# Kernel optimization log

Hardware: AMD Instinct MI355X
Metric: run time of the kernel (lower is better)

Reference implementation:

```python
import jax, jax.numpy as jnp
import numpy as np

B, T, C = 2, 2048, 1280
H, D = 10, 128  # n_head, head_dim (n_kv_head == n_head, so no repeat)
EPS = 1e-5
NEG = -1e9


def setup_inputs() -> dict:
    key = jax.random.key(0)
    ks = jax.random.split(key, 7)
    s = 0.02
    return {
        "x": jax.random.normal(ks[0], (B, T, C), jnp.float32),
        "cos": jax.random.normal(ks[1], (1, 1, T, D // 2), jnp.float32),
        "sin": jax.random.normal(ks[2], (1, 1, T, D // 2), jnp.float32),
        "Wq": jax.random.normal(ks[3], (C, C), jnp.float32) * s,
        "Wk": jax.random.normal(ks[4], (C, C), jnp.float32) * s,
        "Wv": jax.random.normal(ks[5], (C, C), jnp.float32) * s,
        "Wproj": jax.random.normal(ks[6], (C, C), jnp.float32) * s,
    }


def _rope(x, cos, sin):
    # x: [b,h,t,d]; split last dim in half
    x1, x2 = jnp.split(x, 2, axis=-1)
    y1 = x1 * cos + x2 * sin
    y2 = -x1 * sin + x2 * cos
    return jnp.concatenate([y1, y2], axis=-1)


def _rms_norm(x):
    mean = jnp.mean(x * x, axis=-1, keepdims=True)
    return x / jnp.sqrt(mean + EPS)


def reference(x, cos, sin, Wq, Wk, Wv, Wproj):
    b, t, c = x.shape
    # nn.Linear: y = x @ W.T; weights stored [out, in]
    q = (x @ Wq.T).reshape(b, t, H, D).transpose(0, 2, 1, 3)  # [b,h,t,d]
    k = (x @ Wk.T).reshape(b, t, H, D).transpose(0, 2, 1, 3)
    v = (x @ Wv.T).reshape(b, t, H, D).transpose(0, 2, 1, 3)
    q = _rms_norm(_rope(q, cos, sin))
    k = _rms_norm(_rope(k, cos, sin))
    scale = 1.0 / jnp.sqrt(jnp.float32(D))
    scores = jnp.einsum("bhqd,bhkd->bhqk", q, k) * scale
    mask = jnp.triu(jnp.ones((t, t), scores.dtype), k=1)  # 1 above diagonal
    scores = scores + mask * NEG
    attn = jax.nn.softmax(scores, axis=-1)
    y = jnp.einsum("bhqk,bhkd->bhqd", attn, v)
    y = y.transpose(0, 2, 1, 3).reshape(b, t, c)
    return y @ Wproj.T
```

## Files before the change

### kernel.cpp

```cpp
#include <hip/hip_runtime.h>
#include <hip/hip_bf16.h>

#define B_ 2
#define T_ 2048
#define C_ 1280
#define H_ 10
#define D_ 128
#define BT_ (B_*T_)

typedef __hip_bfloat16 bf16;
typedef __attribute__((ext_vector_type(8))) short short8;
typedef __attribute__((ext_vector_type(4))) float f32x4;

__device__ __forceinline__ float bf2f(bf16 v){ return __bfloat162float(v); }
__device__ __forceinline__ bf16  f2bf(float v){ return __float2bfloat16(v); }
__device__ __forceinline__ void stv(bf16* p, float v){ *p = f2bf(v); }
__device__ __forceinline__ void stv(float* p, float v){ *p = v; }

struct alignas(8) bf4 { bf16 a,b,c,d; };

__device__ __forceinline__ void gl2lds(const bf16* g, bf16* l) {
    __builtin_amdgcn_global_load_lds(
        (const __attribute__((address_space(1))) void*)g,
        (__attribute__((address_space(3))) void*)l,
        16, 0, 0);
}

__global__ __launch_bounds__(256)
void cvt(const float* __restrict__ s, bf16* __restrict__ d)
{
    const int i = (blockIdx.x*256 + threadIdx.x)*4;
    const float4 v = *(const float4*)(s + i);
    bf4 o = { f2bf(v.x), f2bf(v.y), f2bf(v.z), f2bf(v.w) };
    *(bf4*)(d + i) = o;
}

__global__ __launch_bounds__(256)
void cvtW(const float* __restrict__ s0, const float* __restrict__ s1,
          const float* __restrict__ s2, const float* __restrict__ s3,
          bf16* __restrict__ d)
{
    const int w = blockIdx.y;
    const float* s = (w==0)?s0:(w==1)?s1:(w==2)?s2:s3;
    const int i = (blockIdx.x*256 + threadIdx.x)*4;
    const float4 v = *(const float4*)(s + i);
    bf4 o = { f2bf(v.x), f2bf(v.y), f2bf(v.z), f2bf(v.w) };
    *(bf4*)(d + (size_t)w*C_*C_ + i) = o;
}

template <typename OT>
__global__ __launch_bounds__(256,4)
void gemm_nt(const bf16* __restrict__ A, const bf16* __restrict__ Wb,
             OT* __restrict__ O0, OT* __restrict__ O1, OT* __restrict__ O2)
{
    __shared__ __align__(16) bf16 As[128*64];
    __shared__ __align__(16) bf16 Bs[128*64];
    const int z = blockIdx.z;
    const bf16* Wm = Wb + (size_t)z*C_*C_;
    OT*         Om = (z==0) ? O0 : (z==1) ? O1 : O2;
    const int wave = threadIdx.x >> 6;
    const int lane = threadIdx.x & 63;
    const int l15 = lane & 15, quad = lane >> 4;
    const int row0 = blockIdx.x*128;
    const int col0 = blockIdx.y*128;
    const int wm = (wave>>1)*64, wn = (wave&1)*64;
    const int srow = lane >> 3;
    const int scol = (lane & 7)*8;

    const f32x4 fzero = {0.f,0.f,0.f,0.f};
    f32x4 acc[4][4];
    #pragma unroll
    for (int i=0;i<4;i++)
        #pragma unroll
        for (int j=0;j<4;j++) acc[i][j] = fzero;

    const bf16* Ag = A  + (size_t)(row0 + wave*32 + srow)*C_ + scol;
    const bf16* Bg = Wm + (size_t)(col0 + wave*32 + srow)*C_ + scol;
    bf16* Al = As + (wave*32)*64;
    bf16* Bl = Bs + (wave*32)*64;

    for (int k0 = 0; k0 < C_; k0 += 64) {
        __syncthreads();
        #pragma unroll
        for (int i=0;i<4;i++){
            gl2lds(Ag + (size_t)i*8*C_ + k0, Al + i*8*64);
            gl2lds(Bg + (size_t)i*8*C_ + k0, Bl + i*8*64);
        }
        asm volatile("s_waitcnt vmcnt(0)" ::: "memory");
        __syncthreads();
        #pragma unroll
        for (int h=0; h<2; ++h) {
            short8 af[4], bfv[4];
            #pragma unroll
            for (int mt=0; mt<4; ++mt) af[mt]  = *(const short8*)(As + (wm + mt*16 + l15)*64 + h*32 + quad*8);
            #pragma unroll
            for (int nt=0; nt<4; ++nt) bfv[nt] = *(const short8*)(Bs + (wn + nt*16 + l15)*64 + h*32 + quad*8);
            #pragma unroll
            for (int mt=0; mt<4; ++mt)
                #pragma unroll
                for (int nt=0; nt<4; ++nt)
                    acc[mt][nt] = __builtin_amdgcn_mfma_f32_16x16x32_bf16(af[mt], bfv[nt], acc[mt][nt], 0,0,0);
        }
    }
    #pragma unroll
    for (int mt=0; mt<4; ++mt)
        #pragma unroll
        for (int nt=0; nt<4; ++nt)
            #pragma unroll
            for (int r=0; r<4; ++r)
                stv(&Om[(size_t)(row0 + wm + mt*16 + quad*4 + r)*C_ + col0 + wn + nt*16 + l15], acc[mt][nt][r]);
}

__global__ __launch_bounds__(256,4)
void gemm_nt_m64(const bf16* __restrict__ A, const bf16* __restrict__ Wm,
                 float* __restrict__ Om)
{
    __shared__ __align__(16) bf16 As[64*64];
    __shared__ __align__(16) bf16 Bs[128*64];
    const int wave = threadIdx.x >> 6;
    const int lane = threadIdx.x & 63;
    const int l15 = lane & 15, quad = lane >> 4;
    const int row0 = blockIdx.x*64;
    const int col0 = blockIdx.y*128;
    const int wm = (wave>>1)*32, wn = (wave&1)*64;
    const int srow = lane >> 3;
    const int scol = (lane & 7)*8;

    const f32x4 fzero = {0.f,0.f,0.f,0.f};
    f32x4 acc[2][4];
    #pragma unroll
    for (int i=0;i<2;i++)
        #pragma unroll
        for (int j=0;j<4;j++) acc[i][j] = fzero;

    const bf16* Ag = A  + (size_t)(row0 + wave*16 + srow)*C_ + scol;
    const bf16* Bg = Wm + (size_t)(col0 + wave*32 + srow)*C_ + scol;
    bf16* Al = As + (wave*16)*64;
    bf16* Bl = Bs + (wave*32)*64;

    for (int k0 = 0; k0 < C_; k0 += 64) {
        __syncthreads();
        #pragma unroll
        for (int i=0;i<2;i++)
            gl2lds(Ag + (size_t)i*8*C_ + k0, Al + i*8*64);
        #pragma unroll
        for (int i=0;i<4;i++)
            gl2lds(Bg + (size_t)i*8*C_ + k0, Bl + i*8*64);
        asm volatile("s_waitcnt vmcnt(0)" ::: "memory");
        __syncthreads();
        #pragma unroll
        for (int h=0; h<2; ++h) {
            short8 af[2], bfv[4];
            #pragma unroll
            for (int mt=0; mt<2; ++mt) af[mt]  = *(const short8*)(As + (wm + mt*16 + l15)*64 + h*32 + quad*8);
            #pragma unroll
            for (int nt=0; nt<4; ++nt) bfv[nt] = *(const short8*)(Bs + (wn + nt*16 + l15)*64 + h*32 + quad*8);
            #pragma unroll
            for (int mt=0; mt<2; ++mt)
                #pragma unroll
                for (int nt=0; nt<4; ++nt)
                    acc[mt][nt] = __builtin_amdgcn_mfma_f32_16x16x32_bf16(af[mt], bfv[nt], acc[mt][nt], 0,0,0);
        }
    }
    #pragma unroll
    for (int mt=0; mt<2; ++mt)
        #pragma unroll
        for (int nt=0; nt<4; ++nt)
            #pragma unroll
            for (int r=0; r<4; ++r)
                Om[(size_t)(row0 + wm + mt*16 + quad*4 + r)*C_ + col0 + wn + nt*16 + l15] = acc[mt][nt][r];
}

__global__ __launch_bounds__(256)
void rope_rms(bf16* __restrict__ q, bf16* __restrict__ k,
              const float* __restrict__ cosp, const float* __restrict__ sinp)
{
    const int wave = threadIdx.x >> 6, lane = threadIdx.x & 63;
    const long rb = (long)blockIdx.x*4 + wave;
    const int h = (int)(rb % H_);
    const long bt = rb / H_;
    const int t = (int)(bt % T_);
    bf16* buf = blockIdx.y ? k : q;
    const size_t base = (size_t)bt*C_ + (size_t)h*D_;
    float x1 = bf2f(buf[base + lane]);
    float x2 = bf2f(buf[base + 64 + lane]);
    float c  = cosp[(size_t)t*64 + lane];
    float s  = sinp[(size_t)t*64 + lane];
    float y1 =  x1*c + x2*s;
    float y2 = -x1*s + x2*c;
    float ss = y1*y1 + y2*y2;
    #pragma unroll
    for (int off=1; off<64; off<<=1) ss += __shfl_xor(ss, off);
    float sc = rsqrtf(ss*(1.0f/128.0f) + 1e-5f);
    buf[base + lane]      = f2bf(y1*sc);
    buf[base + 64 + lane] = f2bf(y2*sc);
}

__global__ __launch_bounds__(256)
void vtrans(const bf16* __restrict__ V, bf16* __restrict__ Vt)
{
    __shared__ float st[64][65];
    const int tid = threadIdx.x;
    const int bh = blockIdx.z;
    const int b = bh / H_, h = bh % H_;
    const int t0 = blockIdx.x*64, d0 = blockIdx.y*64;
    #pragma unroll
    for (int i=0;i<16;i++){
        int e = tid + i*256;
        int r = e >> 6, dd = e & 63;
        st[r][dd] = bf2f(V[(size_t)(b*T_ + t0 + r)*C_ + h*D_ + d0 + dd]);
    }
    __syncthreads();
    #pragma unroll
    for (int i=0;i<16;i++){
        int e = tid + i*256;
        int dd = e >> 6, r = e & 63;
        Vt[((size_t)bh*D_ + d0 + dd)*T_ + t0 + r] = f2bf(st[r][dd]);
    }
}

#define M0_ 11.3137085f
__global__ __launch_bounds__(256,3)
void attn(const bf16* __restrict__ Q, const bf16* __restrict__ K,
          const bf16* __restrict__ Vt, bf16* __restrict__ Y,
          bf16* __restrict__ opart, float* __restrict__ lpart)
{
    __shared__ __align__(16) bf16 kbuf[64*128];
    __shared__ __align__(16) bf16 vbuf[128*64];
    __shared__ __align__(16) bf16 ptile[4][16*72];
    const int wave = threadIdx.x >> 6, lane = threadIdx.x & 63;
    const int l15 = lane & 15, quad = lane >> 4;
    const int bh = blockIdx.x % 20;
    const int u  = blockIdx.x / 20;
    int m, seg;
    if (u < 32)      { m = 31 - (u>>2); seg = u & 3; }
    else if (u < 56) { const int v2 = u-32; m = 23 - v2/3; seg = v2%3; }
    else if (u < 72) { const int v2 = u-56; m = 15 - (v2>>1); seg = v2&1; }
    else             { m = 7 - (u-72); seg = 0; }
    const int b = bh / H_, h = bh % H_;
    const int t0 = m*64;
    const int nch = m + 1;
    const int cbeg = seg*8;
    const int cend = min(cbeg+8, nch);
    const bool direct = (m < 8);
    const size_t base = (size_t)b*T_*C_ + (size_t)h*D_;
    const bf16* Kbh = K + base;
    const bf16* Vbh = Vt + (size_t)bh*D_*T_;
    const int t0w = t0 + wave*16;
    const float scale = 0.08838834764831845f;
    bf16* pt = ptile[wave];

    short8 qa[4];
    {
        const bf16* qp = Q + base + (size_t)(t0w + l15)*C_ + quad*8;
        #pragma unroll
        for (int kb4=0; kb4<4; ++kb4) qa[kb4] = *(const short8*)(qp + kb4*32);
    }
    const f32x4 fzero = {0.f,0.f,0.f,0.f};
    f32x4 o[8];
    #pragma unroll
    for (int dt=0; dt<8; ++dt) o[dt] = fzero;
    float lp[4] = {0.f,0.f,0.f,0.f};

    const int vr_off = lane >> 3;
    const int vu     = lane & 7;

    for (int ch=cbeg; ch<cend; ++ch) {
        const int k0 = ch*64;
        __syncthreads();
        #pragma unroll
        for (int j=0;j<4;j++){
            const int row = wave*16 + j*4 + quad;
            const int ug  = (l15 - row) & 15;
            gl2lds(Kbh + (size_t)(k0 + row)*C_ + ug*8, &kbuf[(wave*16 + j*4)*128]);
        }
        #pragma unroll
        for (int j=0;j<4;j++){
            const int r  = wave*32 + j*8 + vr_off;
            const int ug = (vu - r) & 7;
            gl2lds(Vbh + (size_t)r*T_ + k0 + ug*8, &vbuf[(wave*32 + j*8)*64]);
        }
        asm volatile("s_waitcnt vmcnt(0)" ::: "memory");
        __syncthreads();

        f32x4 sc4[4];
        #pragma unroll
        for (int c=0;c<4;c++) sc4[c] = fzero;
        #pragma unroll
        for (int c=0;c<4;c++){
            short8 kf[4];
            #pragma unroll
            for (int kb4=0; kb4<4; ++kb4) {
                const int up = (kb4*4 + quad + l15) & 15;
                kf[kb4] = *(const short8*)(&kbuf[(c*16 + l15)*128 + up*8]);
            }
            #pragma unroll
            for (int kb4=0; kb4<4; ++kb4)
                sc4[c] = __builtin_amdgcn_mfma_f32_16x16x32_bf16(qa[kb4], kf[kb4], sc4[c], 0,0,0);
        }
        const bool lastc = (ch == nch-1);
        #pragma unroll
        for (int r=0; r<4; ++r) {
            const int rt = t0w + quad*4 + r;
            float v[4];
            #pragma unroll
            for (int c=0;c<4;c++) v[c] = sc4[c][r]*scale;
            if (lastc) {
                #pragma unroll
                for (int c=0;c<4;c++) if (k0 + c*16 + l15 > rt) v[c] = -1e30f;
            }
            float p[4];
            #pragma unroll
            for (int c=0;c<4;c++) p[c] = __expf(v[c] - M0_);
            lp[r] += (p[0]+p[1]) + (p[2]+p[3]);
            #pragma unroll
            for (int c=0;c<4;c++) pt[(quad*4+r)*72 + c*16 + l15] = f2bf(p[c]);
        }
        asm volatile("s_waitcnt lgkmcnt(0)" ::: "memory");
        short8 pa[2];
        #pragma unroll
        for (int ks=0; ks<2; ++ks)
            pa[ks] = *(const short8*)(pt + l15*72 + ks*32 + quad*8);
        #pragma unroll
        for (int dt=0; dt<8; ++dt) {
            #pragma unroll
            for (int ks=0; ks<2; ++ks) {
                const int up = (ks*4 + quad + l15) & 7;
                short8 vF = *(const short8*)(&vbuf[(dt*16 + l15)*64 + up*8]);
                o[dt] = __builtin_amdgcn_mfma_f32_16x16x32_bf16(pa[ks], vF, o[dt], 0,0,0);
            }
        }
    }

    #pragma unroll
    for (int r=0; r<4; ++r) {
        #pragma unroll
        for (int off=1; off<16; off<<=1) lp[r] += __shfl_xor(lp[r], off);
    }
    if (direct) {
        float li[4];
        #pragma unroll
        for (int r=0; r<4; ++r) li[r] = 1.0f/lp[r];
        #pragma unroll
        for (int dt=0; dt<8; ++dt)
            #pragma unroll
            for (int r=0; r<4; ++r)
                Y[base + (size_t)(t0w + quad*4 + r)*C_ + dt*16 + l15] = f2bf(o[dt][r]*li[r]);
    } else {
        const int off = (m<16) ? (m-8)*2 : (m<24) ? 16 + (m-16)*3 : 40 + (m-24)*4;
        const int slot = bh*72 + off + seg;
        bf16* ob = opart + (size_t)slot*8192 + (wave*16)*128;
        #pragma unroll
        for (int dt=0; dt<8; ++dt)
            #pragma unroll
            for (int r=0; r<4; ++r)
                ob[(quad*4+r)*128 + dt*16 + l15] = f2bf(o[dt][r]);
        if (l15 == 0) {
            #pragma unroll
            for (int r=0; r<4; ++r) lpart[(size_t)slot*64 + wave*16 + quad*4 + r] = lp[r];
        }
    }
}

__global__ __launch_bounds__(256)
void combineN(const bf16* __restrict__ opart, const float* __restrict__ lpart,
              bf16* __restrict__ Y)
{
    const int tt = blockIdx.x;
    const int bh = tt / 24;
    const int m  = 8 + (tt % 24);
    const int nseg = (m + 8) >> 3;
    const int off = (m<16) ? (m-8)*2 : (m<24) ? 16 + (m-16)*3 : 40 + (m-24)*4;
    const int slot0 = bh*72 + off;
    const int b = bh / H_, h = bh % H_;
    const int row = threadIdx.x >> 2;
    const int d0 = (threadIdx.x & 3)*32;
    float l = 0.f;
    for (int s=0; s<nseg; ++s) l += lpart[(size_t)(slot0+s)*64 + row];
    const float li = 1.0f/l;
    float acc[32];
    #pragma unroll
    for (int e=0;e<32;e++) acc[e] = 0.f;
    for (int s=0; s<nseg; ++s) {
        const bf16* p = opart + (size_t)(slot0+s)*8192 + row*128 + d0;
        #pragma unroll
        for (int e=0;e<32;e++) acc[e] += bf2f(p[e]);
    }
    bf16 ov[32];
    #pragma unroll
    for (int e=0;e<32;e++) ov[e] = f2bf(acc[e]*li);
    bf16* yp = Y + (size_t)b*T_*C_ + (size_t)(m*64+row)*C_ + (size_t)h*D_ + d0;
    #pragma unroll
    for (int v=0; v<4; ++v) *(short8*)(yp + v*8) = *(const short8*)(&ov[v*8]);
}

extern "C" void kernel_launch(void* const* d_in, const int* in_sizes, int n_in,
                              void* d_out, int out_size, void* d_ws, size_t ws_size,
                              hipStream_t stream)
{
    const float* x    = (const float*)d_in[0];
    const float* cosp = (const float*)d_in[1];
    const float* sinp = (const float*)d_in[2];
    const float* Wq   = (const float*)d_in[3];
    const float* Wk   = (const float*)d_in[4];
    const float* Wv   = (const float*)d_in[5];
    const float* Wp   = (const float*)d_in[6];
    float* out = (float*)d_out;

    const size_t NE = (size_t)BT_ * C_;
    const size_t NW = (size_t)C_ * C_;
    bf16* xb = (bf16*)d_ws;
    bf16* wb = xb + NE;
    bf16* q  = wb + 4*NW;
    bf16* k  = q + NE;
    bf16* v  = k + NE;
    bf16* y  = v + NE;
    bf16* vT = y + NE;
    bf16* op = vT + NE;
    float* lpart = (float*)(op + (size_t)1440*8192);

    cvt<<<dim3(NE/1024), 256, 0, stream>>>(x, xb);
    cvtW<<<dim3(NW/1024, 4), 256, 0, stream>>>(Wq, Wk, Wv, Wp, wb);
    gemm_nt<bf16><<<dim3(BT_/128, C_/128, 3), 256, 0, stream>>>(xb, wb, q, k, v);
    rope_rms<<<dim3(BT_*H_/4, 2), 256, 0, stream>>>(q, k, cosp, sinp);
    vtrans<<<dim3(T_/64, D_/64, B_*H_), 256, 0, stream>>>(v, vT);
    attn<<<dim3(1600), 256, 0, stream>>>(q, k, vT, y, op, lpart);
    combineN<<<dim3(480), 256, 0, stream>>>(op, lpart, y);
    gemm_nt_m64<<<dim3(BT_/64, C_/128), 256, 0, stream>>>(y, wb + 3*NW, out);
}
```

Measured before the change: 246.4 us.

## Replace QKV GEMM with 256x256 double-buffered swizzled tile kernel

New measurement: 249.2 us. Within noise of the previous version (+1.1%).

```diff
diff --git a/kernel.cpp b/kernel.cpp
--- a/kernel.cpp
+++ b/kernel.cpp
@@ -14,8 +14,6 @@
 
 __device__ __forceinline__ float bf2f(bf16 v){ return __bfloat162float(v); }
 __device__ __forceinline__ bf16  f2bf(float v){ return __float2bfloat16(v); }
-__device__ __forceinline__ void stv(bf16* p, float v){ *p = f2bf(v); }
-__device__ __forceinline__ void stv(float* p, float v){ *p = v; }
 
 struct alignas(8) bf4 { bf16 a,b,c,d; };
 
@@ -48,67 +46,140 @@
     *(bf4*)(d + (size_t)w*C_*C_ + i) = o;
 }
 
-template <typename OT>
-__global__ __launch_bounds__(256,4)
-void gemm_nt(const bf16* __restrict__ A, const bf16* __restrict__ Wb,
-             OT* __restrict__ O0, OT* __restrict__ O1, OT* __restrict__ O2)
-{
-    __shared__ __align__(16) bf16 As[128*64];
-    __shared__ __align__(16) bf16 Bs[128*64];
+__global__ __launch_bounds__(512,2)
+void gemm256(const bf16* __restrict__ A, const bf16* __restrict__ Wb,
+             bf16* __restrict__ O0, bf16* __restrict__ O1, bf16* __restrict__ O2)
+{
+    __shared__ __align__(16) bf16 As[2][256*64];
+    __shared__ __align__(16) bf16 Bs[2][256*64];
     const int z = blockIdx.z;
     const bf16* Wm = Wb + (size_t)z*C_*C_;
-    OT*         Om = (z==0) ? O0 : (z==1) ? O1 : O2;
-    const int wave = threadIdx.x >> 6;
+    bf16*       Om = (z==0) ? O0 : (z==1) ? O1 : O2;
+    const int w    = threadIdx.x >> 6;
     const int lane = threadIdx.x & 63;
     const int l15 = lane & 15, quad = lane >> 4;
-    const int row0 = blockIdx.x*128;
-    const int col0 = blockIdx.y*128;
-    const int wm = (wave>>1)*64, wn = (wave&1)*64;
-    const int srow = lane >> 3;
-    const int scol = (lane & 7)*8;
+    const int warp_m = w >> 2, warp_n = w & 3;
+    const int row0 = blockIdx.x*256;
+    const int col0 = blockIdx.y*256;
+
+    const int sr = lane >> 3;
+    const int ug = ((lane & 7) - sr) & 7;
+    const bf16* Ag = A  + (size_t)(row0 + w*32 + sr)*C_ + ug*8;
+    const bf16* Bg = Wm + (size_t)(col0 + w*32 + sr)*C_ + ug*8;
 
     const f32x4 fzero = {0.f,0.f,0.f,0.f};
-    f32x4 acc[4][4];
-    #pragma unroll
-    for (int i=0;i<4;i++)
+    f32x4 acc[8][4];
+    #pragma unroll
+    for (int i=0;i<8;i++)
         #pragma unroll
         for (int j=0;j<4;j++) acc[i][j] = fzero;
 
-    const bf16* Ag = A  + (size_t)(row0 + wave*32 + srow)*C_ + scol;
-    const bf16* Bg = Wm + (size_t)(col0 + wave*32 + srow)*C_ + scol;
-    bf16* Al = As + (wave*32)*64;
-    bf16* Bl = Bs + (wave*32)*64;
-
-    for (int k0 = 0; k0 < C_; k0 += 64) {
+    const int NT = C_/64;
+
+    #pragma unroll
+    for (int tt=0; tt<2; ++tt) {
+        #pragma unroll
+        for (int j=0;j<4;j++){
+            gl2lds(Ag + (size_t)j*8*C_ + tt*64, &As[tt][(w*32 + j*8)*64]);
+            gl2lds(Bg + (size_t)j*8*C_ + tt*64, &Bs[tt][(w*32 + j*8)*64]);
+        }
+    }
+
+    const int arow = warp_m*128 + l15;
+    const int brow = warp_n*64  + l15;
+
+    for (int t=0; t<NT; ++t) {
+        const int cur = t & 1;
+        if (t < NT-1) asm volatile("s_waitcnt vmcnt(8)" ::: "memory");
+        else          asm volatile("s_waitcnt vmcnt(0)" ::: "memory");
         __syncthreads();
+        const bf16* Ab = &As[cur][0];
+        const bf16* Bb = &Bs[cur][0];
+
+        short8 a[4][2], bfr[4][2];
         #pragma unroll
         for (int i=0;i<4;i++){
-            gl2lds(Ag + (size_t)i*8*C_ + k0, Al + i*8*64);
-            gl2lds(Bg + (size_t)i*8*C_ + k0, Bl + i*8*64);
-        }
-        asm volatile("s_waitcnt vmcnt(0)" ::: "memory");
+            const int r = arow + i*16;
+            #pragma unroll
+            for (int h=0;h<2;h++)
+                a[i][h] = *(const short8*)(Ab + r*64 + ((h*4 + quad + r)&7)*8);
+        }
+        #pragma unroll
+        for (int n=0;n<2;n++){
+            const int r = brow + n*16;
+            #pragma unroll
+            for (int h=0;h<2;h++)
+                bfr[n][h] = *(const short8*)(Bb + r*64 + ((h*4 + quad + r)&7)*8);
+        }
+        __builtin_amdgcn_s_setprio(1);
+        #pragma unroll
+        for (int i=0;i<4;i++)
+            #pragma unroll
+            for (int n=0;n<2;n++)
+                #pragma unroll
+                for (int h=0;h<2;h++)
+                    acc[i][n] = __builtin_amdgcn_mfma_f32_16x16x32_bf16(a[i][h], bfr[n][h], acc[i][n], 0,0,0);
+        __builtin_amdgcn_s_setprio(0);
+        #pragma unroll
+        for (int n=2;n<4;n++){
+            const int r = brow + n*16;
+            #pragma unroll
+            for (int h=0;h<2;h++)
+                bfr[n][h] = *(const short8*)(Bb + r*64 + ((h*4 + quad + r)&7)*8);
+        }
+        __builtin_amdgcn_s_setprio(1);
+        #pragma unroll
+        for (int i=0;i<4;i++)
+            #pragma unroll
+            for (int n=2;n<4;n++)
+                #pragma unroll
+                for (int h=0;h<2;h++)
+                    acc[i][n] = __builtin_amdgcn_mfma_f32_16x16x32_bf16(a[i][h], bfr[n][h], acc[i][n], 0,0,0);
+        __builtin_amdgcn_s_setprio(0);
+        #pragma unroll
+        for (int i=0;i<4;i++){
+            const int r = arow + (4+i)*16;
+            #pragma unroll
+            for (int h=0;h<2;h++)
+                a[i][h] = *(const short8*)(Ab + r*64 + ((h*4 + quad + r)&7)*8);
+        }
+        __builtin_amdgcn_s_setprio(1);
+        #pragma unroll
+        for (int i=0;i<4;i++)
+            #pragma unroll
+            for (int n=2;n<4;n++)
+                #pragma unroll
+                for (int h=0;h<2;h++)
+                    acc[4+i][n] = __builtin_amdgcn_mfma_f32_16x16x32_bf16(a[i][h], bfr[n][h], acc[4+i][n], 0,0,0);
+        __builtin_amdgcn_s_setprio(0);
+        __builtin_amdgcn_s_setprio(1);
+        #pragma unroll
+        for (int i=0;i<4;i++)
+            #pragma unroll
+            for (int n=0;n<2;n++)
+                #pragma unroll
+                for (int h=0;h<2;h++)
+                    acc[4+i][n] = __builtin_amdgcn_mfma_f32_16x16x32_bf16(a[i][h], bfr[n][h], acc[4+i][n], 0,0,0);
+        __builtin_amdgcn_s_setprio(0);
+
         __syncthreads();
-        #pragma unroll
-        for (int h=0; h<2; ++h) {
-            short8 af[4], bfv[4];
-            #pragma unroll
-            for (int mt=0; mt<4; ++mt) af[mt]  = *(const short8*)(As + (wm + mt*16 + l15)*64 + h*32 + quad*8);
-            #pragma unroll
-            for (int nt=0; nt<4; ++nt) bfv[nt] = *(const short8*)(Bs + (wn + nt*16 + l15)*64 + h*32 + quad*8);
-            #pragma unroll
-            for (int mt=0; mt<4; ++mt)
-                #pragma unroll
-                for (int nt=0; nt<4; ++nt)
-                    acc[mt][nt] = __builtin_amdgcn_mfma_f32_16x16x32_bf16(af[mt], bfv[nt], acc[mt][nt], 0,0,0);
-        }
-    }
-    #pragma unroll
-    for (int mt=0; mt<4; ++mt)
+        if (t+2 < NT) {
+            #pragma unroll
+            for (int j=0;j<4;j++){
+                gl2lds(Ag + (size_t)j*8*C_ + (t+2)*64, &As[cur][(w*32 + j*8)*64]);
+                gl2lds(Bg + (size_t)j*8*C_ + (t+2)*64, &Bs[cur][(w*32 + j*8)*64]);
+            }
+        }
+    }
+
+    #pragma unroll
+    for (int mt=0; mt<8; ++mt)
         #pragma unroll
         for (int nt=0; nt<4; ++nt)
             #pragma unroll
             for (int r=0; r<4; ++r)
-                stv(&Om[(size_t)(row0 + wm + mt*16 + quad*4 + r)*C_ + col0 + wn + nt*16 + l15], acc[mt][nt][r]);
+                Om[(size_t)(row0 + warp_m*128 + mt*16 + quad*4 + r)*C_ + col0 + warp_n*64 + nt*16 + l15]
+                    = f2bf(acc[mt][nt][r]);
 }
 
 __global__ __launch_bounds__(256,4)
@@ -271,14 +342,14 @@
         #pragma unroll
         for (int j=0;j<4;j++){
             const int row = wave*16 + j*4 + quad;
-            const int ug  = (l15 - row) & 15;
-            gl2lds(Kbh + (size_t)(k0 + row)*C_ + ug*8, &kbuf[(wave*16 + j*4)*128]);
+            const int ugk = (l15 - row) & 15;
+            gl2lds(Kbh + (size_t)(k0 + row)*C_ + ugk*8, &kbuf[(wave*16 + j*4)*128]);
         }
         #pragma unroll
         for (int j=0;j<4;j++){
             const int r  = wave*32 + j*8 + vr_off;
-            const int ug = (vu - r) & 7;
-            gl2lds(Vbh + (size_t)r*T_ + k0 + ug*8, &vbuf[(wave*32 + j*8)*64]);
+            const int ugv = (vu - r) & 7;
+            gl2lds(Vbh + (size_t)r*T_ + k0 + ugv*8, &vbuf[(wave*32 + j*8)*64]);
         }
         asm volatile("s_waitcnt vmcnt(0)" ::: "memory");
         __syncthreads();
@@ -421,7 +492,7 @@
 
     cvt<<<dim3(NE/1024), 256, 0, stream>>>(x, xb);
     cvtW<<<dim3(NW/1024, 4), 256, 0, stream>>>(Wq, Wk, Wv, Wp, wb);
-    gemm_nt<bf16><<<dim3(BT_/128, C_/128, 3), 256, 0, stream>>>(xb, wb, q, k, v);
+    gemm256<<<dim3(BT_/256, C_/256, 3), 512, 0, stream>>>(xb, wb, q, k, v);
     rope_rms<<<dim3(BT_*H_/4, 2), 256, 0, stream>>>(q, k, cosp, sinp);
     vtrans<<<dim3(T_/64, D_/64, B_*H_), 256, 0, stream>>>(v, vT);
     attn<<<dim3(1600), 256, 0, stream>>>(q, k, vT, y, op, lpart);
```

## Fuse RoPE, RMS norm and V transpose into QKV GEMM epilogue

Applied to the files above, without the earlier changes.

Result: faster. 232.3 us (-5.7%).

```diff
diff --git a/kernel.cpp b/kernel.cpp
--- a/kernel.cpp
+++ b/kernel.cpp
@@ -14,8 +14,6 @@
 
 __device__ __forceinline__ float bf2f(bf16 v){ return __bfloat162float(v); }
 __device__ __forceinline__ bf16  f2bf(float v){ return __float2bfloat16(v); }
-__device__ __forceinline__ void stv(bf16* p, float v){ *p = f2bf(v); }
-__device__ __forceinline__ void stv(float* p, float v){ *p = v; }
 
 struct alignas(8) bf4 { bf16 a,b,c,d; };
 
@@ -27,37 +25,38 @@
 }
 
 __global__ __launch_bounds__(256)
-void cvt(const float* __restrict__ s, bf16* __restrict__ d)
-{
-    const int i = (blockIdx.x*256 + threadIdx.x)*4;
+void cvtall(const float* __restrict__ x,  const float* __restrict__ w0,
+            const float* __restrict__ w1, const float* __restrict__ w2,
+            const float* __restrict__ w3, bf16* __restrict__ xb,
+            bf16* __restrict__ wb)
+{
+    int bid = blockIdx.x;
+    const float* s; bf16* d; int i;
+    if (bid < 5120) {
+        s = x; d = xb; i = (bid*256 + threadIdx.x)*4;
+    } else {
+        bid -= 5120;
+        const int w = bid / 1600;
+        const int r = bid % 1600;
+        s = (w==0)?w0:(w==1)?w1:(w==2)?w2:w3;
+        d = wb + (size_t)w*C_*C_;
+        i = (r*256 + threadIdx.x)*4;
+    }
     const float4 v = *(const float4*)(s + i);
     bf4 o = { f2bf(v.x), f2bf(v.y), f2bf(v.z), f2bf(v.w) };
     *(bf4*)(d + i) = o;
 }
 
-__global__ __launch_bounds__(256)
-void cvtW(const float* __restrict__ s0, const float* __restrict__ s1,
-          const float* __restrict__ s2, const float* __restrict__ s3,
-          bf16* __restrict__ d)
-{
-    const int w = blockIdx.y;
-    const float* s = (w==0)?s0:(w==1)?s1:(w==2)?s2:s3;
-    const int i = (blockIdx.x*256 + threadIdx.x)*4;
-    const float4 v = *(const float4*)(s + i);
-    bf4 o = { f2bf(v.x), f2bf(v.y), f2bf(v.z), f2bf(v.w) };
-    *(bf4*)(d + (size_t)w*C_*C_ + i) = o;
-}
-
-template <typename OT>
 __global__ __launch_bounds__(256,4)
-void gemm_nt(const bf16* __restrict__ A, const bf16* __restrict__ Wb,
-             OT* __restrict__ O0, OT* __restrict__ O1, OT* __restrict__ O2)
-{
-    __shared__ __align__(16) bf16 As[128*64];
-    __shared__ __align__(16) bf16 Bs[128*64];
+void gemm_qkv(const bf16* __restrict__ A, const bf16* __restrict__ Wb,
+              bf16* __restrict__ q, bf16* __restrict__ k, bf16* __restrict__ vT,
+              const float* __restrict__ cosp, const float* __restrict__ sinp)
+{
+    __shared__ __align__(16) bf16 smem[17408];
+    bf16* As = smem;
+    bf16* Bs = smem + 8192;
     const int z = blockIdx.z;
     const bf16* Wm = Wb + (size_t)z*C_*C_;
-    OT*         Om = (z==0) ? O0 : (z==1) ? O1 : O2;
     const int wave = threadIdx.x >> 6;
     const int lane = threadIdx.x & 63;
     const int l15 = lane & 15, quad = lane >> 4;
@@ -102,13 +101,92 @@
                     acc[mt][nt] = __builtin_amdgcn_mfma_f32_16x16x32_bf16(af[mt], bfv[nt], acc[mt][nt], 0,0,0);
         }
     }
-    #pragma unroll
-    for (int mt=0; mt<4; ++mt)
-        #pragma unroll
-        for (int nt=0; nt<4; ++nt)
-            #pragma unroll
-            for (int r=0; r<4; ++r)
-                stv(&Om[(size_t)(row0 + wm + mt*16 + quad*4 + r)*C_ + col0 + wn + nt*16 + l15], acc[mt][nt][r]);
+
+    __syncthreads();
+    if (z == 2) {
+        const int RS = 136;
+        #pragma unroll
+        for (int mt=0; mt<4; ++mt)
+            #pragma unroll
+            for (int nt=0; nt<4; ++nt) {
+                bf4 pk = { f2bf(acc[mt][nt][0]), f2bf(acc[mt][nt][1]),
+                           f2bf(acc[mt][nt][2]), f2bf(acc[mt][nt][3]) };
+                *(bf4*)(smem + (wn + nt*16 + l15)*RS + wm + mt*16 + quad*4) = pk;
+            }
+        __syncthreads();
+        const int b    = row0 >> 11;
+        const int trow = row0 & 2047;
+        const int h    = col0 >> 7;
+        bf16* vbase = vT + (size_t)(b*H_ + h)*D_*T_ + trow;
+        const int g   = threadIdx.x >> 4;
+        const int l16 = threadIdx.x & 15;
+        #pragma unroll
+        for (int i=0;i<8;i++){
+            const int col = i*16 + g;
+            *(short8*)(vbase + (size_t)col*T_ + l16*8) = *(const short8*)(smem + col*RS + l16*8);
+        }
+    } else {
+        bf16* dst = z ? k : q;
+        bf16* my  = smem + wave*4096;
+        bf16* pr  = smem + (wave^1)*4096;
+        float* ssb = (float*)(smem + 16384);
+        #pragma unroll
+        for (int mt=0; mt<4; ++mt)
+            #pragma unroll
+            for (int nt=0; nt<4; ++nt) {
+                bf4 pk = { f2bf(acc[mt][nt][0]), f2bf(acc[mt][nt][1]),
+                           f2bf(acc[mt][nt][2]), f2bf(acc[mt][nt][3]) };
+                *(bf4*)(my + ((((mt*4+nt)*4+quad)*16+l15)<<2)) = pk;
+            }
+        __syncthreads();
+        const bool upper = (wave & 1);
+        float ss[4][4];
+        #pragma unroll
+        for (int mt=0; mt<4; ++mt) {
+            #pragma unroll
+            for (int r=0; r<4; ++r) ss[mt][r] = 0.f;
+            #pragma unroll
+            for (int nt=0; nt<4; ++nt) {
+                const bf4 pv = *(const bf4*)(pr + ((((mt*4+nt)*4+quad)*16+l15)<<2));
+                const float p[4] = { bf2f(pv.a), bf2f(pv.b), bf2f(pv.c), bf2f(pv.d) };
+                const int j = nt*16 + l15;
+                #pragma unroll
+                for (int r=0; r<4; ++r) {
+                    const int t = (row0 + wm + mt*16 + quad*4 + r) & 2047;
+                    const float c = cosp[(size_t)t*64 + j];
+                    const float s = sinp[(size_t)t*64 + j];
+                    const float y = upper ? (acc[mt][nt][r]*c - p[r]*s)
+                                          : (acc[mt][nt][r]*c + p[r]*s);
+                    acc[mt][nt][r] = y;
+                    ss[mt][r] += y*y;
+                }
+            }
+            #pragma unroll
+            for (int r=0; r<4; ++r) {
+                #pragma unroll
+                for (int off=1; off<16; off<<=1) ss[mt][r] += __shfl_xor(ss[mt][r], off);
+            }
+        }
+        if (l15 == 0) {
+            #pragma unroll
+            for (int mt=0; mt<4; ++mt)
+                #pragma unroll
+                for (int r=0; r<4; ++r)
+                    ssb[wave*64 + mt*16 + quad*4 + r] = ss[mt][r];
+        }
+        __syncthreads();
+        #pragma unroll
+        for (int mt=0; mt<4; ++mt)
+            #pragma unroll
+            for (int r=0; r<4; ++r) {
+                const float sst = ss[mt][r] + ssb[(wave^1)*64 + mt*16 + quad*4 + r];
+                const float sc = rsqrtf(sst*(1.0f/128.0f) + 1e-5f);
+                #pragma unroll
+                for (int nt=0; nt<4; ++nt)
+                    dst[(size_t)(row0 + wm + mt*16 + quad*4 + r)*C_ + col0 + wn + nt*16 + l15]
+                        = f2bf(acc[mt][nt][r]*sc);
+            }
+    }
 }
 
 __global__ __launch_bounds__(256,4)
@@ -169,54 +247,6 @@
             #pragma unroll
             for (int r=0; r<4; ++r)
                 Om[(size_t)(row0 + wm + mt*16 + quad*4 + r)*C_ + col0 + wn + nt*16 + l15] = acc[mt][nt][r];
-}
-
-__global__ __launch_bounds__(256)
-void rope_rms(bf16* __restrict__ q, bf16* __restrict__ k,
-              const float* __restrict__ cosp, const float* __restrict__ sinp)
-{
-    const int wave = threadIdx.x >> 6, lane = threadIdx.x & 63;
-    const long rb = (long)blockIdx.x*4 + wave;
-    const int h = (int)(rb % H_);
-    const long bt = rb / H_;
-    const int t = (int)(bt % T_);
-    bf16* buf = blockIdx.y ? k : q;
-    const size_t base = (size_t)bt*C_ + (size_t)h*D_;
-    float x1 = bf2f(buf[base + lane]);
-    float x2 = bf2f(buf[base + 64 + lane]);
-    float c  = cosp[(size_t)t*64 + lane];
-    float s  = sinp[(size_t)t*64 + lane];
-    float y1 =  x1*c + x2*s;
-    float y2 = -x1*s + x2*c;
-    float ss = y1*y1 + y2*y2;
-    #pragma unroll
-    for (int off=1; off<64; off<<=1) ss += __shfl_xor(ss, off);
-    float sc = rsqrtf(ss*(1.0f/128.0f) + 1e-5f);
-    buf[base + lane]      = f2bf(y1*sc);
-    buf[base + 64 + lane] = f2bf(y2*sc);
-}
-
-__global__ __launch_bounds__(256)
-void vtrans(const bf16* __restrict__ V, bf16* __restrict__ Vt)
-{
-    __shared__ float st[64][65];
-    const int tid = threadIdx.x;
-    const int bh = blockIdx.z;
-    const int b = bh / H_, h = bh % H_;
-    const int t0 = blockIdx.x*64, d0 = blockIdx.y*64;
-    #pragma unroll
-    for (int i=0;i<16;i++){
-        int e = tid + i*256;
-        int r = e >> 6, dd = e & 63;
-        st[r][dd] = bf2f(V[(size_t)(b*T_ + t0 + r)*C_ + h*D_ + d0 + dd]);
-    }
-    __syncthreads();
-    #pragma unroll
-    for (int i=0;i<16;i++){
-        int e = tid + i*256;
-        int dd = e >> 6, r = e & 63;
-        Vt[((size_t)bh*D_ + d0 + dd)*T_ + t0 + r] = f2bf(st[r][dd]);
-    }
 }
 
 #define M0_ 11.3137085f
@@ -271,14 +301,14 @@
         #pragma unroll
         for (int j=0;j<4;j++){
             const int row = wave*16 + j*4 + quad;
-            const int ug  = (l15 - row) & 15;
-            gl2lds(Kbh + (size_t)(k0 + row)*C_ + ug*8, &kbuf[(wave*16 + j*4)*128]);
+            const int ugk = (l15 - row) & 15;
+            gl2lds(Kbh + (size_t)(k0 + row)*C_ + ugk*8, &kbuf[(wave*16 + j*4)*128]);
         }
         #pragma unroll
         for (int j=0;j<4;j++){
             const int r  = wave*32 + j*8 + vr_off;
-            const int ug = (vu - r) & 7;
-            gl2lds(Vbh + (size_t)r*T_ + k0 + ug*8, &vbuf[(wave*32 + j*8)*64]);
+            const int ugv = (vu - r) & 7;
+            gl2lds(Vbh + (size_t)r*T_ + k0 + ugv*8, &vbuf[(wave*32 + j*8)*64]);
         }
         asm volatile("s_waitcnt vmcnt(0)" ::: "memory");
         __syncthreads();
@@ -419,11 +449,8 @@
     bf16* op = vT + NE;
     float* lpart = (float*)(op + (size_t)1440*8192);
 
-    cvt<<<dim3(NE/1024), 256, 0, stream>>>(x, xb);
-    cvtW<<<dim3(NW/1024, 4), 256, 0, stream>>>(Wq, Wk, Wv, Wp, wb);
-    gemm_nt<bf16><<<dim3(BT_/128, C_/128, 3), 256, 0, stream>>>(xb, wb, q, k, v);
-    rope_rms<<<dim3(BT_*H_/4, 2), 256, 0, stream>>>(q, k, cosp, sinp);
-    vtrans<<<dim3(T_/64, D_/64, B_*H_), 256, 0, stream>>>(v, vT);
+    cvtall<<<dim3(11520), 256, 0, stream>>>(x, Wq, Wk, Wv, Wp, xb, wb);
+    gemm_qkv<<<dim3(BT_/128, C_/128, 3), 256, 0, stream>>>(xb, wb, q, k, vT, cosp, sinp);
     attn<<<dim3(1600), 256, 0, stream>>>(q, k, vT, y, op, lpart);
     combineN<<<dim3(480), 256, 0, stream>>>(op, lpart, y);
     gemm_nt_m64<<<dim3(BT_/64, C_/128), 256, 0, stream>>>(y, wb + 3*NW, out);
```
